# Optimization experiments

Hardware: AMD Instinct MI355X
Metric: run time of the kernel (lower is better)

## Reference

```python
import jax, jax.numpy as jnp
import numpy as np

GROUP = 16
LORA_SCALE = 4.0  # lora_alpha(4*r)/r
EPS = 1e-5


def _dequant(q, scale):
    # q: [O, I] int codes in [0,15]; scale: [O, I//GROUP] per-group normalization
    O, I = q.shape
    s = jnp.repeat(scale, GROUP, axis=1)  # [O, I]
    return (q.astype(jnp.float32) / 15.0 * 2.0 - 1.0) * s


def setup_inputs() -> dict:
    key = jax.random.key(0)
    ks = jax.random.split(key, 6)
    B, D, L, R = 16384, 1024, 18, 32
    x = jax.random.normal(ks[0], (B, D), dtype=jnp.float32)
    q_weights = jax.random.randint(ks[1], (L, D, D), 0, 16, dtype=jnp.int32)
    scales = jax.random.uniform(ks[2], (L, D, D // GROUP), dtype=jnp.float32) * 0.05 + 0.005
    biases = jax.random.normal(ks[3], (L, D), dtype=jnp.float32) * 0.02
    lora_a = jax.random.normal(ks[4], (L, R, D), dtype=jnp.float32) * 0.02
    lora_b = jax.random.normal(ks[5], (L, D, R), dtype=jnp.float32) * 0.02
    ln_gamma = jnp.ones((5, D), dtype=jnp.float32)
    ln_beta = jnp.zeros((5, D), dtype=jnp.float32)
    return {"x": x, "q_weights": q_weights, "scales": scales, "biases": biases,
            "lora_a": lora_a, "lora_b": lora_b, "ln_gamma": ln_gamma, "ln_beta": ln_beta}


def _qlora_linear(x, q, scale, bias, la, lb):
    w = _dequant(q, scale)                       # [O, I]
    base = x @ w.T + bias                        # [B, O]
    lora = (x @ la.T) @ lb.T                     # [B, r] -> [B, O]
    return base + LORA_SCALE * lora


def _layernorm(x, g, b):
    mu = jnp.mean(x, axis=-1, keepdims=True)
    var = jnp.mean(jnp.square(x - mu), axis=-1, keepdims=True)
    return (x - mu) * jax.lax.rsqrt(var + EPS) * g + b


def reference(x, q_weights, scales, biases, lora_a, lora_b, ln_gamma, ln_beta):
    h = x
    for blk in range(6):
        r = h
        for j in range(3):
            li = 3 * blk + j
            r = _qlora_linear(r, q_weights[li], scales[li], biases[li], lora_a[li], lora_b[li])
            if j < 2:
                r = jax.nn.relu(r)
        h = r + h  # residual
        if blk < 5:
            h = _layernorm(h, ln_gamma[blk], ln_beta[blk])
    return h
```

## Files before the change

### kernel.cpp

```cpp
#include <hip/hip_runtime.h>
#include <cstdint>
#include <cstddef>

#define D 1024
#define BATCH 16384
#define NLAYERS 18
#define RR 32

typedef __attribute__((ext_vector_type(8))) __bf16 bf16x8;
typedef __attribute__((ext_vector_type(4))) float f32x4;
typedef __attribute__((address_space(3))) void lds_void_t;
typedef __attribute__((address_space(1))) void gmem_void_t;

__device__ __forceinline__ unsigned short f2bf(float f) {
    unsigned int b = __builtin_bit_cast(unsigned int, f);
    b += 0x7fffu + ((b >> 16) & 1u);
    return (unsigned short)(b >> 16);
}
__device__ __forceinline__ float bf2f(unsigned short u) {
    return __builtin_bit_cast(float, (unsigned int)u << 16);
}

__global__ __launch_bounds__(256) void prep_weights(
    const int* __restrict__ q, const float* __restrict__ scales,
    const float* __restrict__ la, const float* __restrict__ lb,
    unsigned short* __restrict__ weff) {
    __shared__ float la_s[32][260];
    __shared__ float lb_s[64][33];
    __shared__ unsigned short out_s[64][264];
    const int b = blockIdx.x;
    const int li = b >> 6;
    const int o0 = ((b >> 2) & 15) << 6;
    const int i0 = (b & 3) << 8;
    const int t = threadIdx.x;

    {
        const float* src = lb + ((size_t)li * D + o0) * RR;
        for (int i = t; i < 512; i += 256) {
            float4 v = ((const float4*)src)[i];
            const int o = i >> 3, c = (i & 7) << 2;
            lb_s[o][c] = v.x; lb_s[o][c + 1] = v.y; lb_s[o][c + 2] = v.z; lb_s[o][c + 3] = v.w;
        }
    }
    {
        for (int i = t; i < 2048; i += 256) {
            const int r = i >> 6, c = (i & 63) << 2;
            float4 v = *(const float4*)(la + ((size_t)li * RR + r) * D + i0 + c);
            la_s[r][c] = v.x; la_s[r][c + 1] = v.y; la_s[r][c + 2] = v.z; la_s[r][c + 3] = v.w;
        }
    }
    __syncthreads();

    const int ol = t & 63;
    const int ibase = (t >> 6) << 6;
    const size_t grow = (size_t)li * D + o0 + ol;
    float lbr[32];
#pragma unroll
    for (int r = 0; r < 32; ++r) lbr[r] = lb_s[ol][r];

#pragma unroll 1
    for (int iter = 0; iter < 8; ++iter) {
        const int i8 = ibase + (iter << 3);
        const int col = i0 + i8;
        const float s = scales[grow * (D / 16) + (col >> 4)];
        const int* qp = q + grow * D + col;
        int4 q0 = ((const int4*)qp)[0], q1 = ((const int4*)qp)[1];

        float acc[8] = {0.f, 0.f, 0.f, 0.f, 0.f, 0.f, 0.f, 0.f};
#pragma unroll 16
        for (int r = 0; r < 32; ++r) {
            float4 u0 = *(const float4*)&la_s[r][i8];
            float4 u1 = *(const float4*)&la_s[r][i8 + 4];
            const float bv = lbr[r];
            acc[0] += bv * u0.x; acc[1] += bv * u0.y; acc[2] += bv * u0.z; acc[3] += bv * u0.w;
            acc[4] += bv * u1.x; acc[5] += bv * u1.y; acc[6] += bv * u1.z; acc[7] += bv * u1.w;
        }
        int qa[8] = {q0.x, q0.y, q0.z, q0.w, q1.x, q1.y, q1.z, q1.w};
        union { unsigned short us[8]; int4 v; } u;
        const float c = 2.0f / 15.0f;
#pragma unroll
        for (int j = 0; j < 8; ++j)
            u.us[j] = f2bf(((float)qa[j] * c - 1.0f) * s + 4.0f * acc[j]);
        *(int4*)&out_s[ol][i8] = u.v;
    }
    __syncthreads();

    const int row = t >> 2, cg = (t & 3) << 6;
    const size_t gbase = ((size_t)li * D + o0 + row) * D + i0 + cg;
#pragma unroll
    for (int j = 0; j < 8; ++j)
        *(int4*)(weff + gbase + (j << 3)) = *(const int4*)&out_s[row][cg + (j << 3)];
}

__global__ __launch_bounds__(256) void init_h(const float* __restrict__ x,
                                              float* __restrict__ h,
                                              unsigned short* __restrict__ xb) {
    const size_t i = (size_t)blockIdx.x * 256 + threadIdx.x;
    float4 v = ((const float4*)x)[i];
    ((float4*)h)[i] = v;
    ushort4 u;
    u.x = f2bf(v.x); u.y = f2bf(v.y); u.z = f2bf(v.z); u.w = f2bf(v.w);
    ((ushort4*)xb)[i] = u;
}

#define SBAR() do { asm volatile("" ::: "memory"); __builtin_amdgcn_s_barrier(); asm volatile("" ::: "memory"); } while (0)

__global__ __launch_bounds__(512, 2) void gemm256(
    const unsigned short* __restrict__ xb, const unsigned short* __restrict__ w,
    const float* __restrict__ bias,
    unsigned short* __restrict__ outb, int mode) {
    __shared__ __align__(16) char smem[131072];
    const int tid = threadIdx.x;
    const int wid = tid >> 6, lane = tid & 63;
    const int bid = blockIdx.x + (blockIdx.y << 2);
    const int xcd = bid & 7, slot = bid >> 3;
    const int m0 = ((xcd << 3) + (slot >> 2)) << 8;
    const int n0 = (slot & 3) << 8;
    const int l15 = lane & 15, kgrp = lane >> 4;
    const int wrow = (wid >> 2) << 7;
    const int wcol = (wid & 3) << 6;

    f32x4 acc[8][4];
#pragma unroll
    for (int i = 0; i < 8; ++i)
#pragma unroll
        for (int j = 0; j < 4; ++j) acc[i][j] = 0.0f;

#define STAGE_HALF(hs, i_)                                                     \
    do {                                                                       \
        const int k0_ = (hs) << 5;                                             \
        char* sA_ = smem + ((hs) & 3) * 32768;                                 \
        const int off_ = (i_) * 8192 + (tid << 4);                             \
        const int r_ = off_ >> 6;                                              \
        const int j_ = ((off_ >> 4) & 3) ^ ((r_ >> 1) & 3);                    \
        const unsigned short* ga_ = xb + (size_t)(m0 + r_) * D + k0_ + (j_ << 3); \
        const unsigned short* gb_ = w + (size_t)(n0 + r_) * D + k0_ + (j_ << 3);  \
        char* lA_ = sA_ + (i_) * 8192 + (wid << 10);                           \
        __builtin_amdgcn_global_load_lds((const gmem_void_t*)ga_, (lds_void_t*)lA_, 16, 0, 0);          \
        __builtin_amdgcn_global_load_lds((const gmem_void_t*)gb_, (lds_void_t*)(lA_ + 16384), 16, 0, 0); \
    } while (0)

    STAGE_HALF(0, 0); STAGE_HALF(0, 1);
    STAGE_HALF(1, 0); STAGE_HALF(1, 1);
    STAGE_HALF(2, 0); STAGE_HALF(2, 1);
    asm volatile("s_waitcnt vmcnt(8)" ::: "memory");
    SBAR();

    for (int h = 0; h < 32; ++h) {
        const char* sA = smem + (h & 3) * 32768;
        const char* sB = sA + 16384;
        bf16x8 a[8], b[4];
#pragma unroll
        for (int f = 0; f < 4; ++f) {
            const int r = wrow + (f << 4) + l15;
            a[f] = *(const bf16x8*)(sA + (r << 6) + ((kgrp ^ ((r >> 1) & 3)) << 4));
        }
#pragma unroll
        for (int g = 0; g < 4; ++g) {
            const int r = wcol + (g << 4) + l15;
            b[g] = *(const bf16x8*)(sB + (r << 6) + ((kgrp ^ ((r >> 1) & 3)) << 4));
        }
        if (h < 29) STAGE_HALF(h + 3, 0);
        SBAR();
        asm volatile("s_waitcnt lgkmcnt(0)" ::: "memory");
        __builtin_amdgcn_s_setprio(1);
#pragma unroll
        for (int mi = 0; mi < 4; ++mi)
#pragma unroll
            for (int ni = 0; ni < 4; ++ni)
                acc[mi][ni] = __builtin_amdgcn_mfma_f32_16x16x32_bf16(
                    a[mi], b[ni], acc[mi][ni], 0, 0, 0);
        __builtin_amdgcn_s_setprio(0);
        SBAR();
#pragma unroll
        for (int f = 4; f < 8; ++f) {
            const int r = wrow + (f << 4) + l15;
            a[f] = *(const bf16x8*)(sA + (r << 6) + ((kgrp ^ ((r >> 1) & 3)) << 4));
        }
        if (h < 29) {
            STAGE_HALF(h + 3, 1);
            asm volatile("s_waitcnt vmcnt(8)" ::: "memory");
        } else if (h == 29) {
            asm volatile("s_waitcnt vmcnt(4)" ::: "memory");
        } else if (h == 30) {
            asm volatile("s_waitcnt vmcnt(0)" ::: "memory");
        }
        SBAR();
        asm volatile("s_waitcnt lgkmcnt(0)" ::: "memory");
        __builtin_amdgcn_s_setprio(1);
#pragma unroll
        for (int mi = 4; mi < 8; ++mi)
#pragma unroll
            for (int ni = 0; ni < 4; ++ni)
                acc[mi][ni] = __builtin_amdgcn_mfma_f32_16x16x32_bf16(
                    a[mi], b[ni], acc[mi][ni], 0, 0, 0);
        __builtin_amdgcn_s_setprio(0);
        SBAR();
    }

    const int crow = kgrp << 2;
    float bv[4];
#pragma unroll
    for (int ni = 0; ni < 4; ++ni) bv[ni] = bias[n0 + wcol + (ni << 4) + l15];
#pragma unroll
    for (int mi = 0; mi < 8; ++mi) {
        const int rbase = m0 + wrow + (mi << 4) + crow;
#pragma unroll
        for (int ni = 0; ni < 4; ++ni) {
            const int col = n0 + wcol + (ni << 4) + l15;
#pragma unroll
            for (int r = 0; r < 4; ++r) {
                float v = acc[mi][ni][r] + bv[ni];
                if (mode == 0) v = v > 0.0f ? v : 0.0f;
                outb[(size_t)(rbase + r) * D + col] = f2bf(v);
            }
        }
    }
}

__global__ __launch_bounds__(256) void resid_ln_v(
    float* __restrict__ h, const unsigned short* __restrict__ vb,
    unsigned short* __restrict__ xb,
    const float* __restrict__ gamma, const float* __restrict__ beta) {
    const int row = blockIdx.x;
    const int t = threadIdx.x;
    float* hr = h + (size_t)row * D;
    float4 v = ((float4*)hr)[t];
    ushort4 vv = ((const ushort4*)(vb + (size_t)row * D))[t];
    v.x += bf2f(vv.x); v.y += bf2f(vv.y); v.z += bf2f(vv.z); v.w += bf2f(vv.w);
    float s = v.x + v.y + v.z + v.w;
    float s2 = v.x * v.x + v.y * v.y + v.z * v.z + v.w * v.w;
#pragma unroll
    for (int off = 32; off > 0; off >>= 1) {
        s += __shfl_down(s, off);
        s2 += __shfl_down(s2, off);
    }
    __shared__ float red[8];
    const int wid = t >> 6, lane = t & 63;
    if (lane == 0) { red[wid] = s; red[wid + 4] = s2; }
    __syncthreads();
    s = red[0] + red[1] + red[2] + red[3];
    s2 = red[4] + red[5] + red[6] + red[7];
    const float mu = s * (1.0f / D);
    const float var = s2 * (1.0f / D) - mu * mu;
    const float rs = rsqrtf(var + 1e-5f);
    float4 g = ((const float4*)gamma)[t];
    float4 b = ((const float4*)beta)[t];
    float4 o;
    o.x = (v.x - mu) * rs * g.x + b.x;
    o.y = (v.y - mu) * rs * g.y + b.y;
    o.z = (v.z - mu) * rs * g.z + b.z;
    o.w = (v.w - mu) * rs * g.w + b.w;
    ((float4*)hr)[t] = o;
    ushort4 u;
    u.x = f2bf(o.x); u.y = f2bf(o.y); u.z = f2bf(o.z); u.w = f2bf(o.w);
    ((ushort4*)(xb + (size_t)row * D))[t] = u;
}

__global__ __launch_bounds__(256) void final_add(
    const float* __restrict__ h, const unsigned short* __restrict__ vb,
    float* __restrict__ out) {
    const size_t i = (size_t)blockIdx.x * 256 + threadIdx.x;
    float4 hv = ((const float4*)h)[i];
    ushort4 vv = ((const ushort4*)vb)[i];
    float4 o;
    o.x = hv.x + bf2f(vv.x); o.y = hv.y + bf2f(vv.y);
    o.z = hv.z + bf2f(vv.z); o.w = hv.w + bf2f(vv.w);
    ((float4*)out)[i] = o;
}

extern "C" void kernel_launch(void* const* d_in, const int* in_sizes, int n_in,
                              void* d_out, int out_size, void* d_ws, size_t ws_size,
                              hipStream_t stream) {
    const float* x      = (const float*)d_in[0];
    const int*   q      = (const int*)d_in[1];
    const float* scales = (const float*)d_in[2];
    const float* biases = (const float*)d_in[3];
    const float* la     = (const float*)d_in[4];
    const float* lb     = (const float*)d_in[5];
    const float* lng    = (const float*)d_in[6];
    const float* lnb    = (const float*)d_in[7];
    float* out = (float*)d_out;

    char* p = (char*)d_ws;
    unsigned short* weff = (unsigned short*)p; p += (size_t)NLAYERS * D * D * 2;
    unsigned short* xbA  = (unsigned short*)p; p += (size_t)BATCH * D * 2;
    unsigned short* xbB  = (unsigned short*)p; p += (size_t)BATCH * D * 2;
    float*          h    = (float*)p;

    prep_weights<<<NLAYERS * 16 * 4, 256, 0, stream>>>(q, scales, la, lb, weff);
    init_h<<<BATCH * D / 4 / 256, 256, 0, stream>>>(x, h, xbA);

    dim3 ggrid(D / 256, BATCH / 256);
    for (int blk = 0; blk < 6; ++blk) {
        const int li = 3 * blk;
        gemm256<<<ggrid, 512, 0, stream>>>(xbA, weff + (size_t)li * D * D,
                                           biases + (size_t)li * D, xbB, 0);
        gemm256<<<ggrid, 512, 0, stream>>>(xbB, weff + (size_t)(li + 1) * D * D,
                                           biases + (size_t)(li + 1) * D, xbA, 0);
        gemm256<<<ggrid, 512, 0, stream>>>(xbA, weff + (size_t)(li + 2) * D * D,
                                           biases + (size_t)(li + 2) * D, xbB, 1);
        if (blk < 5)
            resid_ln_v<<<BATCH, 256, 0, stream>>>(h, xbB, xbA,
                                                  lng + (size_t)blk * D, lnb + (size_t)blk * D);
        else
            final_add<<<BATCH * D / 4 / 256, 256, 0, stream>>>(h, xbB, out);
    }
}
```

Before: 940.2 us.

## Switch GEMM to 32x32x16 MFMA with k-chunk LDS layout and split prep_weights

The main GEMM now uses 32x32x16 bf16 MFMA tiles instead of 16x16x32. The LDS staging layout is reorganized into per-k-chunk column-major blocks, so each lane reads one contiguous 16-byte row slice without XOR swizzling, and A and B are staged in separate halves of each iteration. The aim is fewer MFMA issues and LDS reads per FLOP. prep_weights now computes the LoRA product into LDS first, then does a coalesced dequant-and-write pass straight to global memory. That pass rounds the LoRA term to bf16 before the add, which adds a small extra precision loss.

```diff
diff --git a/kernel.cpp b/kernel.cpp
--- a/kernel.cpp
+++ b/kernel.cpp
@@ -9,6 +9,7 @@
 
 typedef __attribute__((ext_vector_type(8))) __bf16 bf16x8;
 typedef __attribute__((ext_vector_type(4))) float f32x4;
+typedef __attribute__((ext_vector_type(16))) float f32x16;
 typedef __attribute__((address_space(3))) void lds_void_t;
 typedef __attribute__((address_space(1))) void gmem_void_t;
 
@@ -27,7 +28,7 @@
     unsigned short* __restrict__ weff) {
     __shared__ float la_s[32][260];
     __shared__ float lb_s[64][33];
-    __shared__ unsigned short out_s[64][264];
+    __shared__ unsigned short lo_s[64][264];
     const int b = blockIdx.x;
     const int li = b >> 6;
     const int o0 = ((b >> 2) & 15) << 6;
@@ -51,45 +52,52 @@
     }
     __syncthreads();
 
-    const int ol = t & 63;
-    const int ibase = (t >> 6) << 6;
-    const size_t grow = (size_t)li * D + o0 + ol;
-    float lbr[32];
-#pragma unroll
-    for (int r = 0; r < 32; ++r) lbr[r] = lb_s[ol][r];
+    {
+        const int ol = t & 63;
+        const int ibase = (t >> 6) << 6;
+        float lbr[32];
+#pragma unroll
+        for (int r = 0; r < 32; ++r) lbr[r] = lb_s[ol][r];
+#pragma unroll 1
+        for (int iter = 0; iter < 8; ++iter) {
+            const int i8 = ibase + (iter << 3);
+            float acc[8] = {0.f, 0.f, 0.f, 0.f, 0.f, 0.f, 0.f, 0.f};
+#pragma unroll 16
+            for (int r = 0; r < 32; ++r) {
+                float4 u0 = *(const float4*)&la_s[r][i8];
+                float4 u1 = *(const float4*)&la_s[r][i8 + 4];
+                const float bv = lbr[r];
+                acc[0] += bv * u0.x; acc[1] += bv * u0.y; acc[2] += bv * u0.z; acc[3] += bv * u0.w;
+                acc[4] += bv * u1.x; acc[5] += bv * u1.y; acc[6] += bv * u1.z; acc[7] += bv * u1.w;
+            }
+            union { unsigned short us[8]; int4 v; } u;
+#pragma unroll
+            for (int j = 0; j < 8; ++j) u.us[j] = f2bf(4.0f * acc[j]);
+            *(int4*)&lo_s[ol][i8] = u.v;
+        }
+    }
+    __syncthreads();
 
 #pragma unroll 1
     for (int iter = 0; iter < 8; ++iter) {
-        const int i8 = ibase + (iter << 3);
+        const int cidx = t + (iter << 8);
+        const int row = cidx >> 5;
+        const int i8 = (cidx & 31) << 3;
+        const size_t grow = (size_t)li * D + o0 + row;
         const int col = i0 + i8;
         const float s = scales[grow * (D / 16) + (col >> 4)];
         const int* qp = q + grow * D + col;
         int4 q0 = ((const int4*)qp)[0], q1 = ((const int4*)qp)[1];
-
-        float acc[8] = {0.f, 0.f, 0.f, 0.f, 0.f, 0.f, 0.f, 0.f};
-#pragma unroll 16
-        for (int r = 0; r < 32; ++r) {
-            float4 u0 = *(const float4*)&la_s[r][i8];
-            float4 u1 = *(const float4*)&la_s[r][i8 + 4];
-            const float bv = lbr[r];
-            acc[0] += bv * u0.x; acc[1] += bv * u0.y; acc[2] += bv * u0.z; acc[3] += bv * u0.w;
-            acc[4] += bv * u1.x; acc[5] += bv * u1.y; acc[6] += bv * u1.z; acc[7] += bv * u1.w;
-        }
+        union { unsigned short us[8]; int4 v; } lo;
+        lo.v = *(const int4*)&lo_s[row][i8];
         int qa[8] = {q0.x, q0.y, q0.z, q0.w, q1.x, q1.y, q1.z, q1.w};
         union { unsigned short us[8]; int4 v; } u;
         const float c = 2.0f / 15.0f;
 #pragma unroll
         for (int j = 0; j < 8; ++j)
-            u.us[j] = f2bf(((float)qa[j] * c - 1.0f) * s + 4.0f * acc[j]);
-        *(int4*)&out_s[ol][i8] = u.v;
-    }
-    __syncthreads();
-
-    const int row = t >> 2, cg = (t & 3) << 6;
-    const size_t gbase = ((size_t)li * D + o0 + row) * D + i0 + cg;
-#pragma unroll
-    for (int j = 0; j < 8; ++j)
-        *(int4*)(weff + gbase + (j << 3)) = *(const int4*)&out_s[row][cg + (j << 3)];
+            u.us[j] = f2bf(((float)qa[j] * c - 1.0f) * s + bf2f(lo.us[j]));
+        *(int4*)(weff + grow * D + col) = u.v;
+    }
 }
 
 __global__ __launch_bounds__(256) void init_h(const float* __restrict__ x,
@@ -116,69 +124,87 @@
     const int xcd = bid & 7, slot = bid >> 3;
     const int m0 = ((xcd << 3) + (slot >> 2)) << 8;
     const int n0 = (slot & 3) << 8;
-    const int l15 = lane & 15, kgrp = lane >> 4;
+    const int l31 = lane & 31, khalf = lane >> 5;
     const int wrow = (wid >> 2) << 7;
     const int wcol = (wid & 3) << 6;
 
-    f32x4 acc[8][4];
-#pragma unroll
-    for (int i = 0; i < 8; ++i)
-#pragma unroll
-        for (int j = 0; j < 4; ++j) acc[i][j] = 0.0f;
-
-#define STAGE_HALF(hs, i_)                                                     \
+    f32x16 acc[4][2];
+#pragma unroll
+    for (int i = 0; i < 4; ++i)
+#pragma unroll
+        for (int j = 0; j < 2; ++j) acc[i][j] = 0.0f;
+
+    const int sc_ = wid & 3;
+    const int sg_ = (wid >> 2) << 1;
+
+#define STAGE_A(hs)                                                            \
     do {                                                                       \
-        const int k0_ = (hs) << 5;                                             \
-        char* sA_ = smem + ((hs) & 3) * 32768;                                 \
-        const int off_ = (i_) * 8192 + (tid << 4);                             \
-        const int r_ = off_ >> 6;                                              \
-        const int j_ = ((off_ >> 4) & 3) ^ ((r_ >> 1) & 3);                    \
-        const unsigned short* ga_ = xb + (size_t)(m0 + r_) * D + k0_ + (j_ << 3); \
-        const unsigned short* gb_ = w + (size_t)(n0 + r_) * D + k0_ + (j_ << 3);  \
-        char* lA_ = sA_ + (i_) * 8192 + (wid << 10);                           \
-        __builtin_amdgcn_global_load_lds((const gmem_void_t*)ga_, (lds_void_t*)lA_, 16, 0, 0);          \
-        __builtin_amdgcn_global_load_lds((const gmem_void_t*)gb_, (lds_void_t*)(lA_ + 16384), 16, 0, 0); \
+        char* base_ = smem + ((hs) & 3) * 32768;                               \
+        const int k0_ = ((hs) << 5) + (sc_ << 3);                              \
+        _Pragma("unroll")                                                      \
+        for (int i_ = 0; i_ < 2; ++i_) {                                       \
+            const int row_ = ((sg_ + i_) << 6) + lane;                         \
+            const unsigned short* ga_ = xb + (size_t)(m0 + row_) * D + k0_;    \
+            char* dst_ = base_ + (sc_ << 12) + ((sg_ + i_) << 10);             \
+            __builtin_amdgcn_global_load_lds((const gmem_void_t*)ga_, (lds_void_t*)dst_, 16, 0, 0); \
+        }                                                                      \
     } while (0)
 
-    STAGE_HALF(0, 0); STAGE_HALF(0, 1);
-    STAGE_HALF(1, 0); STAGE_HALF(1, 1);
-    STAGE_HALF(2, 0); STAGE_HALF(2, 1);
+#define STAGE_B(hs)                                                            \
+    do {                                                                       \
+        char* base_ = smem + ((hs) & 3) * 32768 + 16384;                       \
+        const int k0_ = ((hs) << 5) + (sc_ << 3);                              \
+        _Pragma("unroll")                                                      \
+        for (int i_ = 0; i_ < 2; ++i_) {                                       \
+            const int row_ = ((sg_ + i_) << 6) + lane;                         \
+            const unsigned short* gb_ = w + (size_t)(n0 + row_) * D + k0_;     \
+            char* dst_ = base_ + (sc_ << 12) + ((sg_ + i_) << 10);             \
+            __builtin_amdgcn_global_load_lds((const gmem_void_t*)gb_, (lds_void_t*)dst_, 16, 0, 0); \
+        }                                                                      \
+    } while (0)
+
+    STAGE_A(0); STAGE_B(0);
+    STAGE_A(1); STAGE_B(1);
+    STAGE_A(2); STAGE_B(2);
     asm volatile("s_waitcnt vmcnt(8)" ::: "memory");
     SBAR();
 
     for (int h = 0; h < 32; ++h) {
         const char* sA = smem + (h & 3) * 32768;
         const char* sB = sA + 16384;
-        bf16x8 a[8], b[4];
-#pragma unroll
-        for (int f = 0; f < 4; ++f) {
-            const int r = wrow + (f << 4) + l15;
-            a[f] = *(const bf16x8*)(sA + (r << 6) + ((kgrp ^ ((r >> 1) & 3)) << 4));
-        }
-#pragma unroll
-        for (int g = 0; g < 4; ++g) {
-            const int r = wcol + (g << 4) + l15;
-            b[g] = *(const bf16x8*)(sB + (r << 6) + ((kgrp ^ ((r >> 1) & 3)) << 4));
-        }
-        if (h < 29) STAGE_HALF(h + 3, 0);
+        bf16x8 a[4], b[2];
+        {
+            const int rc = khalf << 12;
+#pragma unroll
+            for (int f = 0; f < 4; ++f)
+                a[f] = *(const bf16x8*)(sA + rc + ((wrow + (f << 5) + l31) << 4));
+#pragma unroll
+            for (int g = 0; g < 2; ++g)
+                b[g] = *(const bf16x8*)(sB + rc + ((wcol + (g << 5) + l31) << 4));
+        }
+        if (h < 29) STAGE_A(h + 3);
         SBAR();
         asm volatile("s_waitcnt lgkmcnt(0)" ::: "memory");
         __builtin_amdgcn_s_setprio(1);
 #pragma unroll
         for (int mi = 0; mi < 4; ++mi)
 #pragma unroll
-            for (int ni = 0; ni < 4; ++ni)
-                acc[mi][ni] = __builtin_amdgcn_mfma_f32_16x16x32_bf16(
+            for (int ni = 0; ni < 2; ++ni)
+                acc[mi][ni] = __builtin_amdgcn_mfma_f32_32x32x16_bf16(
                     a[mi], b[ni], acc[mi][ni], 0, 0, 0);
         __builtin_amdgcn_s_setprio(0);
         SBAR();
-#pragma unroll
-        for (int f = 4; f < 8; ++f) {
-            const int r = wrow + (f << 4) + l15;
-            a[f] = *(const bf16x8*)(sA + (r << 6) + ((kgrp ^ ((r >> 1) & 3)) << 4));
+        {
+            const int rc = (khalf + 2) << 12;
+#pragma unroll
+            for (int f = 0; f < 4; ++f)
+                a[f] = *(const bf16x8*)(sA + rc + ((wrow + (f << 5) + l31) << 4));
+#pragma unroll
+            for (int g = 0; g < 2; ++g)
+                b[g] = *(const bf16x8*)(sB + rc + ((wcol + (g << 5) + l31) << 4));
         }
         if (h < 29) {
-            STAGE_HALF(h + 3, 1);
+            STAGE_B(h + 3);
             asm volatile("s_waitcnt vmcnt(8)" ::: "memory");
         } else if (h == 29) {
             asm volatile("s_waitcnt vmcnt(4)" ::: "memory");
@@ -189,30 +215,31 @@
         asm volatile("s_waitcnt lgkmcnt(0)" ::: "memory");
         __builtin_amdgcn_s_setprio(1);
 #pragma unroll
-        for (int mi = 4; mi < 8; ++mi)
-#pragma unroll
-            for (int ni = 0; ni < 4; ++ni)
-                acc[mi][ni] = __builtin_amdgcn_mfma_f32_16x16x32_bf16(
+        for (int mi = 0; mi < 4; ++mi)
+#pragma unroll
+            for (int ni = 0; ni < 2; ++ni)
+                acc[mi][ni] = __builtin_amdgcn_mfma_f32_32x32x16_bf16(
                     a[mi], b[ni], acc[mi][ni], 0, 0, 0);
         __builtin_amdgcn_s_setprio(0);
         SBAR();
     }
 
-    const int crow = kgrp << 2;
-    float bv[4];
-#pragma unroll
-    for (int ni = 0; ni < 4; ++ni) bv[ni] = bias[n0 + wcol + (ni << 4) + l15];
-#pragma unroll
-    for (int mi = 0; mi < 8; ++mi) {
-        const int rbase = m0 + wrow + (mi << 4) + crow;
-#pragma unroll
-        for (int ni = 0; ni < 4; ++ni) {
-            const int col = n0 + wcol + (ni << 4) + l15;
-#pragma unroll
-            for (int r = 0; r < 4; ++r) {
-                float v = acc[mi][ni][r] + bv[ni];
+    const int colbase = n0 + wcol + l31;
+    const float bv0 = bias[colbase];
+    const float bv1 = bias[colbase + 32];
+#pragma unroll
+    for (int mi = 0; mi < 4; ++mi) {
+        const int rbase = m0 + wrow + (mi << 5) + (khalf << 2);
+#pragma unroll
+        for (int ni = 0; ni < 2; ++ni) {
+            const float bv = ni ? bv1 : bv0;
+            const int col = colbase + (ni << 5);
+#pragma unroll
+            for (int reg = 0; reg < 16; ++reg) {
+                const int row = rbase + (reg & 3) + ((reg >> 2) << 3);
+                float v = acc[mi][ni][reg] + bv;
                 if (mode == 0) v = v > 0.0f ? v : 0.0f;
-                outb[(size_t)(rbase + r) * D + col] = f2bf(v);
+                outb[(size_t)row * D + col] = f2bf(v);
             }
         }
     }
```

Measured after the change: 1.017 ms. +8.2%, slower.

## Split weight prep into MFMA LoRA product kernel and streaming dequant kernel

Applied to the files above, without the earlier changes.

Weight preparation used to compute the rank-32 LoRA product lb·la with scalar FP32 FMAs inside the dequant kernel. It is now two kernels. The first computes the LoRA delta for each layer with bf16 MFMA tiles and writes it as bf16 into the h buffer, which is unused at that point. The second is a grid-stride streaming kernel that dequantizes the int4 codes and adds the stored delta. This moves the outer product onto matrix cores but adds an extra bf16 round-trip of the delta through memory, rounds la and lb to bf16 first, and uses uncoalesced scalar stores in the LoRA kernel.

```diff
diff --git a/kernel.cpp b/kernel.cpp
--- a/kernel.cpp
+++ b/kernel.cpp
@@ -12,6 +12,8 @@
 typedef __attribute__((address_space(3))) void lds_void_t;
 typedef __attribute__((address_space(1))) void gmem_void_t;
 
+union bfpack { unsigned short us[8]; int4 v; };
+
 __device__ __forceinline__ unsigned short f2bf(float f) {
     unsigned int b = __builtin_bit_cast(unsigned int, f);
     b += 0x7fffu + ((b >> 16) & 1u);
@@ -21,75 +23,102 @@
     return __builtin_bit_cast(float, (unsigned int)u << 16);
 }
 
-__global__ __launch_bounds__(256) void prep_weights(
-    const int* __restrict__ q, const float* __restrict__ scales,
+__global__ __launch_bounds__(512) void lora_gemm(
     const float* __restrict__ la, const float* __restrict__ lb,
-    unsigned short* __restrict__ weff) {
-    __shared__ float la_s[32][260];
-    __shared__ float lb_s[64][33];
-    __shared__ unsigned short out_s[64][264];
+    unsigned short* __restrict__ loraB) {
+    __shared__ unsigned short lbs[256][40];
+    __shared__ unsigned short lat[256][40];
     const int b = blockIdx.x;
-    const int li = b >> 6;
-    const int o0 = ((b >> 2) & 15) << 6;
+    const int li = b >> 4;
+    const int o0 = ((b >> 2) & 3) << 8;
     const int i0 = (b & 3) << 8;
     const int t = threadIdx.x;
 
     {
-        const float* src = lb + ((size_t)li * D + o0) * RR;
-        for (int i = t; i < 512; i += 256) {
-            float4 v = ((const float4*)src)[i];
-            const int o = i >> 3, c = (i & 7) << 2;
-            lb_s[o][c] = v.x; lb_s[o][c + 1] = v.y; lb_s[o][c + 2] = v.z; lb_s[o][c + 3] = v.w;
-        }
+        const int row = t >> 1, half = t & 1;
+        const float* src = lb + ((size_t)(li * D) + o0 + row) * RR + half * 16;
+        bfpack u[2];
+#pragma unroll
+        for (int j = 0; j < 2; ++j) {
+            float4 v0 = ((const float4*)src)[2 * j];
+            float4 v1 = ((const float4*)src)[2 * j + 1];
+            u[j].us[0] = f2bf(v0.x); u[j].us[1] = f2bf(v0.y);
+            u[j].us[2] = f2bf(v0.z); u[j].us[3] = f2bf(v0.w);
+            u[j].us[4] = f2bf(v1.x); u[j].us[5] = f2bf(v1.y);
+            u[j].us[6] = f2bf(v1.z); u[j].us[7] = f2bf(v1.w);
+        }
+        *(int4*)&lbs[row][half * 16] = u[0].v;
+        *(int4*)&lbs[row][half * 16 + 8] = u[1].v;
     }
     {
-        for (int i = t; i < 2048; i += 256) {
-            const int r = i >> 6, c = (i & 63) << 2;
-            float4 v = *(const float4*)(la + ((size_t)li * RR + r) * D + i0 + c);
-            la_s[r][c] = v.x; la_s[r][c + 1] = v.y; la_s[r][c + 2] = v.z; la_s[r][c + 3] = v.w;
+        const int col = t >> 1, rhalf = t & 1;
+#pragma unroll
+        for (int rr = 0; rr < 16; ++rr) {
+            const int r = rhalf * 16 + rr;
+            lat[col][r] = f2bf(la[((size_t)li * RR + r) * D + i0 + col]);
         }
     }
     __syncthreads();
 
-    const int ol = t & 63;
-    const int ibase = (t >> 6) << 6;
-    const size_t grow = (size_t)li * D + o0 + ol;
-    float lbr[32];
-#pragma unroll
-    for (int r = 0; r < 32; ++r) lbr[r] = lb_s[ol][r];
-
-#pragma unroll 1
-    for (int iter = 0; iter < 8; ++iter) {
-        const int i8 = ibase + (iter << 3);
-        const int col = i0 + i8;
-        const float s = scales[grow * (D / 16) + (col >> 4)];
-        const int* qp = q + grow * D + col;
+    const int wid = t >> 6, lane = t & 63;
+    const int l15 = lane & 15, kgrp = lane >> 4;
+    const int wrow = (wid >> 2) << 7;
+    const int wcol = (wid & 3) << 6;
+
+    bf16x8 a[8], bb[4];
+#pragma unroll
+    for (int f = 0; f < 8; ++f)
+        a[f] = *(const bf16x8*)&lbs[wrow + (f << 4) + l15][kgrp << 3];
+#pragma unroll
+    for (int g = 0; g < 4; ++g)
+        bb[g] = *(const bf16x8*)&lat[wcol + (g << 4) + l15][kgrp << 3];
+
+    f32x4 acc[8][4];
+#pragma unroll
+    for (int i = 0; i < 8; ++i)
+#pragma unroll
+        for (int j = 0; j < 4; ++j) acc[i][j] = 0.0f;
+#pragma unroll
+    for (int mi = 0; mi < 8; ++mi)
+#pragma unroll
+        for (int ni = 0; ni < 4; ++ni)
+            acc[mi][ni] = __builtin_amdgcn_mfma_f32_16x16x32_bf16(
+                a[mi], bb[ni], acc[mi][ni], 0, 0, 0);
+
+    unsigned short* dst = loraB + (size_t)li * D * D;
+#pragma unroll
+    for (int mi = 0; mi < 8; ++mi) {
+        const int row = o0 + wrow + (mi << 4) + (kgrp << 2);
+#pragma unroll
+        for (int ni = 0; ni < 4; ++ni) {
+            const int col = i0 + wcol + (ni << 4) + l15;
+#pragma unroll
+            for (int r = 0; r < 4; ++r)
+                dst[(size_t)(row + r) * D + col] = f2bf(4.0f * acc[mi][ni][r]);
+        }
+    }
+}
+
+__global__ __launch_bounds__(256) void dequant(
+    const int* __restrict__ q, const float* __restrict__ scales,
+    const unsigned short* __restrict__ loraB, unsigned short* __restrict__ weff) {
+    const size_t n8 = (size_t)NLAYERS * D * D / 8;
+    const float c = 2.0f / 15.0f;
+    for (size_t i = (size_t)blockIdx.x * 256 + threadIdx.x; i < n8;
+         i += (size_t)gridDim.x * 256) {
+        const size_t base = i << 3;
+        const int* qp = q + base;
         int4 q0 = ((const int4*)qp)[0], q1 = ((const int4*)qp)[1];
-
-        float acc[8] = {0.f, 0.f, 0.f, 0.f, 0.f, 0.f, 0.f, 0.f};
-#pragma unroll 16
-        for (int r = 0; r < 32; ++r) {
-            float4 u0 = *(const float4*)&la_s[r][i8];
-            float4 u1 = *(const float4*)&la_s[r][i8 + 4];
-            const float bv = lbr[r];
-            acc[0] += bv * u0.x; acc[1] += bv * u0.y; acc[2] += bv * u0.z; acc[3] += bv * u0.w;
-            acc[4] += bv * u1.x; acc[5] += bv * u1.y; acc[6] += bv * u1.z; acc[7] += bv * u1.w;
-        }
+        bfpack lo;
+        lo.v = *(const int4*)(loraB + base);
+        const float s = scales[base >> 4];
         int qa[8] = {q0.x, q0.y, q0.z, q0.w, q1.x, q1.y, q1.z, q1.w};
-        union { unsigned short us[8]; int4 v; } u;
-        const float c = 2.0f / 15.0f;
+        bfpack u;
 #pragma unroll
         for (int j = 0; j < 8; ++j)
-            u.us[j] = f2bf(((float)qa[j] * c - 1.0f) * s + 4.0f * acc[j]);
-        *(int4*)&out_s[ol][i8] = u.v;
-    }
-    __syncthreads();
-
-    const int row = t >> 2, cg = (t & 3) << 6;
-    const size_t gbase = ((size_t)li * D + o0 + row) * D + i0 + cg;
-#pragma unroll
-    for (int j = 0; j < 8; ++j)
-        *(int4*)(weff + gbase + (j << 3)) = *(const int4*)&out_s[row][cg + (j << 3)];
+            u.us[j] = f2bf(((float)qa[j] * c - 1.0f) * s + bf2f(lo.us[j]));
+        *(int4*)(weff + base) = u.v;
+    }
 }
 
 __global__ __launch_bounds__(256) void init_h(const float* __restrict__ x,
@@ -287,8 +316,10 @@
     unsigned short* xbA  = (unsigned short*)p; p += (size_t)BATCH * D * 2;
     unsigned short* xbB  = (unsigned short*)p; p += (size_t)BATCH * D * 2;
     float*          h    = (float*)p;
-
-    prep_weights<<<NLAYERS * 16 * 4, 256, 0, stream>>>(q, scales, la, lb, weff);
+    unsigned short* loraB = (unsigned short*)h;
+
+    lora_gemm<<<NLAYERS * 16, 512, 0, stream>>>(la, lb, loraB);
+    dequant<<<2048, 256, 0, stream>>>(q, scales, loraB, weff);
     init_h<<<BATCH * D / 4 / 256, 256, 0, stream>>>(x, h, xbA);
 
     dim3 ggrid(D / 256, BATCH / 256);
```

New measurement: 902.4 us. 1.04x faster.

## Keep residual stream in bf16 and compute LoRA weight delta with MFMA

Applied to the files above, without the earlier changes.

Removes the fp32 residual buffer h. The residual and layernorm output are now kept only as a bf16 activation buffer, with a third ping-pong buffer so the block input survives the three GEMMs. This cuts memory traffic in the layernorm and final-add kernels and drops the fp32 copy in init. The weight prep now computes the LoRA product lb@la with bf16 MFMA instead of scalar fp32 FMAs, and writes dequantized rows directly to global memory. The trade-off is lower precision in the residual path and in the LoRA delta.

```diff
diff --git a/kernel.cpp b/kernel.cpp
--- a/kernel.cpp
+++ b/kernel.cpp
@@ -12,6 +12,8 @@
 typedef __attribute__((address_space(3))) void lds_void_t;
 typedef __attribute__((address_space(1))) void gmem_void_t;
 
+union bfpack { unsigned short us[8]; int4 v; };
+
 __device__ __forceinline__ unsigned short f2bf(float f) {
     unsigned int b = __builtin_bit_cast(unsigned int, f);
     b += 0x7fffu + ((b >> 16) & 1u);
@@ -21,12 +23,12 @@
     return __builtin_bit_cast(float, (unsigned int)u << 16);
 }
 
-__global__ __launch_bounds__(256) void prep_weights(
+__global__ __launch_bounds__(256) void lora_dequant(
+    const float* __restrict__ la, const float* __restrict__ lb,
     const int* __restrict__ q, const float* __restrict__ scales,
-    const float* __restrict__ la, const float* __restrict__ lb,
     unsigned short* __restrict__ weff) {
-    __shared__ float la_s[32][260];
-    __shared__ float lb_s[64][33];
+    __shared__ unsigned short lbs[64][40];
+    __shared__ unsigned short lat[256][40];
     __shared__ unsigned short out_s[64][264];
     const int b = blockIdx.x;
     const int li = b >> 6;
@@ -35,69 +37,84 @@
     const int t = threadIdx.x;
 
     {
-        const float* src = lb + ((size_t)li * D + o0) * RR;
-        for (int i = t; i < 512; i += 256) {
-            float4 v = ((const float4*)src)[i];
-            const int o = i >> 3, c = (i & 7) << 2;
-            lb_s[o][c] = v.x; lb_s[o][c + 1] = v.y; lb_s[o][c + 2] = v.z; lb_s[o][c + 3] = v.w;
-        }
+        const int row = t >> 2, qt = t & 3;
+        const float* src = lb + ((size_t)(li * D) + o0 + row) * RR + qt * 8;
+        float4 v0 = ((const float4*)src)[0], v1 = ((const float4*)src)[1];
+        bfpack u;
+        u.us[0] = f2bf(v0.x); u.us[1] = f2bf(v0.y); u.us[2] = f2bf(v0.z); u.us[3] = f2bf(v0.w);
+        u.us[4] = f2bf(v1.x); u.us[5] = f2bf(v1.y); u.us[6] = f2bf(v1.z); u.us[7] = f2bf(v1.w);
+        *(int4*)&lbs[row][qt * 8] = u.v;
     }
     {
-        for (int i = t; i < 2048; i += 256) {
-            const int r = i >> 6, c = (i & 63) << 2;
-            float4 v = *(const float4*)(la + ((size_t)li * RR + r) * D + i0 + c);
-            la_s[r][c] = v.x; la_s[r][c + 1] = v.y; la_s[r][c + 2] = v.z; la_s[r][c + 3] = v.w;
-        }
+        const int col = t;
+#pragma unroll 8
+        for (int r = 0; r < 32; ++r)
+            lat[col][r] = f2bf(la[((size_t)li * RR + r) * D + i0 + col]);
     }
     __syncthreads();
 
-    const int ol = t & 63;
-    const int ibase = (t >> 6) << 6;
-    const size_t grow = (size_t)li * D + o0 + ol;
-    float lbr[32];
-#pragma unroll
-    for (int r = 0; r < 32; ++r) lbr[r] = lb_s[ol][r];
-
+    {
+        const int wid = t >> 6, lane = t & 63;
+        const int l15 = lane & 15, kgrp = lane >> 4;
+        const int wrow = (wid >> 1) << 5;
+        const int wcol = (wid & 1) << 7;
+        bf16x8 a[2], bb[8];
+#pragma unroll
+        for (int f = 0; f < 2; ++f)
+            a[f] = *(const bf16x8*)&lbs[wrow + (f << 4) + l15][kgrp << 3];
+#pragma unroll
+        for (int g = 0; g < 8; ++g)
+            bb[g] = *(const bf16x8*)&lat[wcol + (g << 4) + l15][kgrp << 3];
+        f32x4 acc[2][8];
+#pragma unroll
+        for (int i = 0; i < 2; ++i)
+#pragma unroll
+            for (int j = 0; j < 8; ++j) acc[i][j] = 0.0f;
+#pragma unroll
+        for (int mi = 0; mi < 2; ++mi)
+#pragma unroll
+            for (int ni = 0; ni < 8; ++ni)
+                acc[mi][ni] = __builtin_amdgcn_mfma_f32_16x16x32_bf16(
+                    a[mi], bb[ni], acc[mi][ni], 0, 0, 0);
+#pragma unroll
+        for (int mi = 0; mi < 2; ++mi) {
+            const int row = wrow + (mi << 4) + (kgrp << 2);
+#pragma unroll
+            for (int ni = 0; ni < 8; ++ni) {
+                const int col = wcol + (ni << 4) + l15;
+#pragma unroll
+                for (int r = 0; r < 4; ++r)
+                    out_s[row + r][col] = f2bf(4.0f * acc[mi][ni][r]);
+            }
+        }
+    }
+    __syncthreads();
+
+    const float c = 2.0f / 15.0f;
 #pragma unroll 1
     for (int iter = 0; iter < 8; ++iter) {
-        const int i8 = ibase + (iter << 3);
-        const int col = i0 + i8;
+        const int idx = (iter << 8) + t;
+        const int row = idx >> 5, c8 = (idx & 31) << 3;
+        const size_t grow = (size_t)li * D + o0 + row;
+        const int col = i0 + c8;
         const float s = scales[grow * (D / 16) + (col >> 4)];
         const int* qp = q + grow * D + col;
         int4 q0 = ((const int4*)qp)[0], q1 = ((const int4*)qp)[1];
-
-        float acc[8] = {0.f, 0.f, 0.f, 0.f, 0.f, 0.f, 0.f, 0.f};
-#pragma unroll 16
-        for (int r = 0; r < 32; ++r) {
-            float4 u0 = *(const float4*)&la_s[r][i8];
-            float4 u1 = *(const float4*)&la_s[r][i8 + 4];
-            const float bv = lbr[r];
-            acc[0] += bv * u0.x; acc[1] += bv * u0.y; acc[2] += bv * u0.z; acc[3] += bv * u0.w;
-            acc[4] += bv * u1.x; acc[5] += bv * u1.y; acc[6] += bv * u1.z; acc[7] += bv * u1.w;
-        }
+        bfpack lo;
+        lo.v = *(const int4*)&out_s[row][c8];
         int qa[8] = {q0.x, q0.y, q0.z, q0.w, q1.x, q1.y, q1.z, q1.w};
-        union { unsigned short us[8]; int4 v; } u;
-        const float c = 2.0f / 15.0f;
+        bfpack u;
 #pragma unroll
         for (int j = 0; j < 8; ++j)
-            u.us[j] = f2bf(((float)qa[j] * c - 1.0f) * s + 4.0f * acc[j]);
-        *(int4*)&out_s[ol][i8] = u.v;
-    }
-    __syncthreads();
-
-    const int row = t >> 2, cg = (t & 3) << 6;
-    const size_t gbase = ((size_t)li * D + o0 + row) * D + i0 + cg;
-#pragma unroll
-    for (int j = 0; j < 8; ++j)
-        *(int4*)(weff + gbase + (j << 3)) = *(const int4*)&out_s[row][cg + (j << 3)];
-}
-
-__global__ __launch_bounds__(256) void init_h(const float* __restrict__ x,
-                                              float* __restrict__ h,
-                                              unsigned short* __restrict__ xb) {
+            u.us[j] = f2bf(((float)qa[j] * c - 1.0f) * s + bf2f(lo.us[j]));
+        *(int4*)(weff + grow * D + col) = u.v;
+    }
+}
+
+__global__ __launch_bounds__(256) void init_xb(const float* __restrict__ x,
+                                               unsigned short* __restrict__ xb) {
     const size_t i = (size_t)blockIdx.x * 256 + threadIdx.x;
     float4 v = ((const float4*)x)[i];
-    ((float4*)h)[i] = v;
     ushort4 u;
     u.x = f2bf(v.x); u.y = f2bf(v.y); u.z = f2bf(v.z); u.w = f2bf(v.w);
     ((ushort4*)xb)[i] = u;
@@ -218,16 +235,17 @@
     }
 }
 
-__global__ __launch_bounds__(256) void resid_ln_v(
-    float* __restrict__ h, const unsigned short* __restrict__ vb,
-    unsigned short* __restrict__ xb,
+__global__ __launch_bounds__(256) void resid_ln_b(
+    unsigned short* __restrict__ hb, const unsigned short* __restrict__ vb,
     const float* __restrict__ gamma, const float* __restrict__ beta) {
     const int row = blockIdx.x;
     const int t = threadIdx.x;
-    float* hr = h + (size_t)row * D;
-    float4 v = ((float4*)hr)[t];
+    unsigned short* hr = hb + (size_t)row * D;
+    ushort4 hv = ((const ushort4*)hr)[t];
     ushort4 vv = ((const ushort4*)(vb + (size_t)row * D))[t];
-    v.x += bf2f(vv.x); v.y += bf2f(vv.y); v.z += bf2f(vv.z); v.w += bf2f(vv.w);
+    float4 v;
+    v.x = bf2f(hv.x) + bf2f(vv.x); v.y = bf2f(hv.y) + bf2f(vv.y);
+    v.z = bf2f(hv.z) + bf2f(vv.z); v.w = bf2f(hv.w) + bf2f(vv.w);
     float s = v.x + v.y + v.z + v.w;
     float s2 = v.x * v.x + v.y * v.y + v.z * v.z + v.w * v.w;
 #pragma unroll
@@ -246,26 +264,23 @@
     const float rs = rsqrtf(var + 1e-5f);
     float4 g = ((const float4*)gamma)[t];
     float4 b = ((const float4*)beta)[t];
-    float4 o;
-    o.x = (v.x - mu) * rs * g.x + b.x;
-    o.y = (v.y - mu) * rs * g.y + b.y;
-    o.z = (v.z - mu) * rs * g.z + b.z;
-    o.w = (v.w - mu) * rs * g.w + b.w;
-    ((float4*)hr)[t] = o;
     ushort4 u;
-    u.x = f2bf(o.x); u.y = f2bf(o.y); u.z = f2bf(o.z); u.w = f2bf(o.w);
-    ((ushort4*)(xb + (size_t)row * D))[t] = u;
+    u.x = f2bf((v.x - mu) * rs * g.x + b.x);
+    u.y = f2bf((v.y - mu) * rs * g.y + b.y);
+    u.z = f2bf((v.z - mu) * rs * g.z + b.z);
+    u.w = f2bf((v.w - mu) * rs * g.w + b.w);
+    ((ushort4*)hr)[t] = u;
 }
 
 __global__ __launch_bounds__(256) void final_add(
-    const float* __restrict__ h, const unsigned short* __restrict__ vb,
+    const unsigned short* __restrict__ hb, const unsigned short* __restrict__ vb,
     float* __restrict__ out) {
     const size_t i = (size_t)blockIdx.x * 256 + threadIdx.x;
-    float4 hv = ((const float4*)h)[i];
+    ushort4 hv = ((const ushort4*)hb)[i];
     ushort4 vv = ((const ushort4*)vb)[i];
     float4 o;
-    o.x = hv.x + bf2f(vv.x); o.y = hv.y + bf2f(vv.y);
-    o.z = hv.z + bf2f(vv.z); o.w = hv.w + bf2f(vv.w);
+    o.x = bf2f(hv.x) + bf2f(vv.x); o.y = bf2f(hv.y) + bf2f(vv.y);
+    o.z = bf2f(hv.z) + bf2f(vv.z); o.w = bf2f(hv.w) + bf2f(vv.w);
     ((float4*)out)[i] = o;
 }
 
@@ -286,10 +301,10 @@
     unsigned short* weff = (unsigned short*)p; p += (size_t)NLAYERS * D * D * 2;
     unsigned short* xbA  = (unsigned short*)p; p += (size_t)BATCH * D * 2;
     unsigned short* xbB  = (unsigned short*)p; p += (size_t)BATCH * D * 2;
-    float*          h    = (float*)p;
-
-    prep_weights<<<NLAYERS * 16 * 4, 256, 0, stream>>>(q, scales, la, lb, weff);
-    init_h<<<BATCH * D / 4 / 256, 256, 0, stream>>>(x, h, xbA);
+    unsigned short* xbC  = (unsigned short*)p;
+
+    lora_dequant<<<NLAYERS * 16 * 4, 256, 0, stream>>>(la, lb, q, scales, weff);
+    init_xb<<<BATCH * D / 4 / 256, 256, 0, stream>>>(x, xbA);
 
     dim3 ggrid(D / 256, BATCH / 256);
     for (int blk = 0; blk < 6; ++blk) {
@@ -297,13 +312,13 @@
         gemm256<<<ggrid, 512, 0, stream>>>(xbA, weff + (size_t)li * D * D,
                                            biases + (size_t)li * D, xbB, 0);
         gemm256<<<ggrid, 512, 0, stream>>>(xbB, weff + (size_t)(li + 1) * D * D,
-                                           biases + (size_t)(li + 1) * D, xbA, 0);
-        gemm256<<<ggrid, 512, 0, stream>>>(xbA, weff + (size_t)(li + 2) * D * D,
+                                           biases + (size_t)(li + 1) * D, xbC, 0);
+        gemm256<<<ggrid, 512, 0, stream>>>(xbC, weff + (size_t)(li + 2) * D * D,
                                            biases + (size_t)(li + 2) * D, xbB, 1);
         if (blk < 5)
-            resid_ln_v<<<BATCH, 256, 0, stream>>>(h, xbB, xbA,
+            resid_ln_b<<<BATCH, 256, 0, stream>>>(xbA, xbB,
                                                   lng + (size_t)blk * D, lnb + (size_t)blk * D);
         else
-            final_add<<<BATCH * D / 4 / 256, 256, 0, stream>>>(h, xbB, out);
-    }
-}
+            final_add<<<BATCH * D / 4 / 256, 256, 0, stream>>>(xbA, xbB, out);
+    }
+}
```

Result: faster. 849.7 us (-9.6%).
